# Performance work log

Hardware: AMD Instinct MI355X
Metric: run time of the kernel (lower is better)

The kernel has to match this reference:

```python
import jax, jax.numpy as jnp
import numpy as np

KERNELS = ("gaussian", "laplacian", "gaussian", "laplacian")
N, M, D, N_PER = 384, 384, 64, 200


def setup_inputs():
    key = jax.random.key(0)
    kx, ky, kb, kp = jax.random.split(key, 4)
    X = jax.random.normal(kx, (N, D), dtype=jnp.float32)
    Y = jax.random.normal(ky, (M, D), dtype=jnp.float32)
    # positive bandwidths of realistic magnitude for d=64 gaussian/laplacian kernels
    bandwidths = jax.random.uniform(kb, (4,), dtype=jnp.float32) * 8.0 + 4.0
    # each row is a random permutation of n+m indices (torch.randperm equivalent)
    perms = jax.vmap(lambda k: jax.random.permutation(k, N + M))(
        jax.random.split(kp, N_PER)).astype(jnp.int32)
    return {"X": X, "Y": Y, "bandwidths": bandwidths, "perms": perms}


def _pairwise_dist(Z):
    # torch.cdist(Z, Z, p=2); eps keeps sqrt grad finite on the zero diagonal
    sq = jnp.sum(Z * Z, axis=1)
    d2 = jnp.maximum(sq[:, None] + sq[None, :] - 2.0 * (Z @ Z.T), 0.0)
    return jnp.sqrt(d2 + 1e-12)


def reference(X, Y, bandwidths, perms):
    n, m = X.shape[0], Y.shape[0]
    Z = jnp.concatenate([X, Y], axis=0)            # [n+m, d]
    dist = _pairwise_dist(Z)                        # [n+m, n+m]
    idx = jnp.arange(min(n, m))
    perm_X, perm_Y = perms[:, :n], perms[:, n:]    # [n_per, n], [n_per, m]
    U, U_b = [], []
    for i, kern in enumerate(KERNELS):
        b = bandwidths[i]
        if kern == "gaussian":
            K = jnp.exp(-(dist * dist) / (b * b))
        else:  # laplacian
            K = jnp.exp(-dist / b)
        # mmd_u's in-place K_XY[diag]=0 mutates the view of K, so zero first
        K = K.at[idx, n + idx].set(0.0)
        K_XX, K_YY, K_XY = K[:n, :n], K[n:, n:], K[:n, n:]
        mmd = ((K_XX.sum() - jnp.trace(K_XX)) / (n * (n - 1))
               + (K_YY.sum() - jnp.trace(K_YY)) / (m * (m - 1))
               - 2.0 * K_XY.sum() / (n * m))
        U.append(mmd)
        # fast_perm: gather permuted blocks, zero diagonals, reduce per permutation
        diagK = jnp.diagonal(K)
        sXX = K[perm_X[:, :, None], perm_X[:, None, :]].sum((1, 2)) - diagK[perm_X].sum(1)
        sYY = K[perm_Y[:, :, None], perm_Y[:, None, :]].sum((1, 2)) - diagK[perm_Y].sum(1)
        sXY = (K[perm_X[:, :, None], perm_Y[:, None, :]].sum((1, 2))
               - K[perm_X[:, idx], perm_Y[:, idx]].sum(1))
        U_b.append(sXX / (n * (n - 1)) + sYY / (m * (m - 1)) - 2.0 * sXY / (n * m))
    U = jnp.stack(U)[:, None]    # [n_b, 1]  == compute_U_stats U.unsqueeze(1)
    U_b = jnp.stack(U_b)         # [n_b, n_per]
    return jnp.concatenate([U, U_b], axis=1)  # [n_b, 1 + n_per]
```

## Files before the change

### kernel.cpp

```cpp
#include <hip/hip_runtime.h>

#define NTOT 768
#define NHALF 384
#define DDIM 64
#define NPER 200
#define PPAD 256
#define NKER 4
#define CHUNK 192
#define NMB 12
#define NB_GEMM 192

typedef __attribute__((ext_vector_type(8))) short short8;
typedef __attribute__((ext_vector_type(4))) float floatx4;

constexpr int K0SZ  = NTOT * NTOT;
constexpr int OF_KH = 0;
constexpr int KH_FLOATS = NKER * K0SZ / 2;
constexpr int OF_RS0 = OF_KH + KH_FLOATS;
constexpr int OF_RSX = OF_RS0 + NKER * NTOT;
constexpr int OF_RSY = OF_RSX + NKER * NTOT;
constexpr int OF_C   = OF_RSY + NKER * NTOT;
constexpr int OF_ROWM = OF_C + NKER * NHALF;
constexpr int OF_COLM = OF_ROWM + NKER * NTOT;
constexpr int OF_SCAL = OF_COLM + NKER * NTOT;
constexpr int OF_STT  = OF_SCAL + 16;
constexpr int STT_FLOATS = PPAD * NTOT / 2;
constexpr int OF_Q0P  = OF_STT + STT_FLOATS;

constexpr int SMEMF = CHUNK * 65 + 2 * DDIM + 64;

__device__ __forceinline__ unsigned short f2bf(float f) {
    unsigned int u = __float_as_uint(f);
    return (unsigned short)((u + 0x7FFFu + ((u >> 16) & 1u)) >> 16);
}
__device__ __forceinline__ float bf2f(unsigned short h) {
    return __uint_as_float(((unsigned int)h) << 16);
}

__global__ __launch_bounds__(256) void k_s1(const float* __restrict__ X,
                                            const float* __restrict__ Y,
                                            const float* __restrict__ bw,
                                            const int* __restrict__ perms,
                                            float* __restrict__ ws) {
    __shared__ float smem[SMEMF];
    float* zb   = smem;
    float* zaS  = smem + CHUNK * 65;
    float* redw = zaS + 2 * DDIM;
    int bid = blockIdx.x, tid = threadIdx.x;
    int wave = tid >> 6, lane = tid & 63;
    unsigned short* STT = (unsigned short*)(ws + OF_STT);
    unsigned short* KH  = (unsigned short*)(ws + OF_KH);

    if (bid < NPER) {
        if (tid < 192) {
            ((uint2*)(STT + bid * NTOT))[tid] = make_uint2(0u, 0u);
            if (bid < PPAD - NPER)
                ((uint2*)(STT + (NPER + bid) * NTOT))[tid] = make_uint2(0u, 0u);
        }
        __syncthreads();
        int v = perms[bid * NTOT + tid];
        STT[bid * NTOT + v] = 0x3F80;
        if (tid < NHALF - 256) {
            int v2 = perms[bid * NTOT + 256 + tid];
            STT[bid * NTOT + v2] = 0x3F80;
        }
        return;
    }

    int a0 = bid - NPER;
    int a1 = a0 + NHALF;
    if (tid < DDIM)               zaS[tid] = X[a0 * DDIM + tid];
    else if (tid < 2 * DDIM)      zaS[tid] = Y[a0 * DDIM + (tid - DDIM)];
    float ib2[NKER], ib1[NKER];
#pragma unroll
    for (int k = 0; k < NKER; ++k) { float b = bw[k]; ib2[k] = 1.f / (b * b); ib1[k] = 1.f / b; }
    __syncthreads();
    float sq0 = 0.f, sq1 = 0.f;
#pragma unroll
    for (int d = 0; d < DDIM; ++d) {
        sq0 = fmaf(zaS[d], zaS[d], sq0);
        sq1 = fmaf(zaS[DDIM + d], zaS[DDIM + d], sq1);
    }
    float acc[16];
#pragma unroll
    for (int j = 0; j < 16; ++j) acc[j] = 0.f;

    for (int c0 = 0; c0 < NTOT; c0 += CHUNK) {
        __syncthreads();
        for (int idx = tid; idx < CHUNK * DDIM; idx += 256) {
            int r = idx >> 6, d = idx & 63;
            int gr = c0 + r;
            const float* zr = (gr < NHALF) ? X + gr * DDIM : Y + (gr - NHALF) * DDIM;
            zb[r * 65 + d] = zr[d];
        }
        __syncthreads();
        if (tid < CHUNK) {
            int b = c0 + tid;
            float dot0 = 0.f, dot1 = 0.f, sqb = 0.f;
#pragma unroll
            for (int d = 0; d < DDIM; ++d) {
                float zv = zb[tid * 65 + d];
                dot0 = fmaf(zaS[d], zv, dot0);
                dot1 = fmaf(zaS[DDIM + d], zv, dot1);
                sqb  = fmaf(zv, zv, sqb);
            }
            {
                float d2 = (sq0 + sqb) - 2.f * dot0;
                if (b == a0) d2 = 0.f;
                d2 = fmaxf(d2, 0.f);
                float d2e = d2 + 1e-12f;
                float dist = sqrtf(d2e);
#pragma unroll
                for (int k = 0; k < NKER; ++k) {
                    float val = ((k & 1) == 0) ? __expf(-d2e * ib2[k]) : __expf(-dist * ib1[k]);
                    KH[k * K0SZ + a0 * NTOT + b] = f2bf(val);
                    if (b < NHALF) acc[k] += val; else acc[4 + k] += val;
                    if (b == a0 + NHALF) ws[OF_C + k * NHALF + a0] = val;
                }
            }
            {
                float d2 = (sq1 + sqb) - 2.f * dot1;
                if (b == a1) d2 = 0.f;
                d2 = fmaxf(d2, 0.f);
                float d2e = d2 + 1e-12f;
                float dist = sqrtf(d2e);
#pragma unroll
                for (int k = 0; k < NKER; ++k) {
                    float val = ((k & 1) == 0) ? __expf(-d2e * ib2[k]) : __expf(-dist * ib1[k]);
                    KH[k * K0SZ + a1 * NTOT + b] = f2bf(val);
                    if (b < NHALF) acc[8 + k] += val; else acc[12 + k] += val;
                }
            }
        }
    }
#pragma unroll
    for (int off = 32; off > 0; off >>= 1)
#pragma unroll
        for (int j = 0; j < 16; ++j) acc[j] += __shfl_down(acc[j], off, 64);
    __syncthreads();
    if (lane == 0)
#pragma unroll
        for (int j = 0; j < 16; ++j) redw[wave * 16 + j] = acc[j];
    __syncthreads();
    if (tid == 0) {
#pragma unroll
        for (int k = 0; k < NKER; ++k) {
            float sx0 = redw[k]      + redw[16 + k]      + redw[32 + k]      + redw[48 + k];
            float sy0 = redw[4 + k]  + redw[20 + k]      + redw[36 + k]      + redw[52 + k];
            float sx1 = redw[8 + k]  + redw[24 + k]      + redw[40 + k]      + redw[56 + k];
            float sy1 = redw[12 + k] + redw[28 + k]      + redw[44 + k]      + redw[60 + k];
            ws[OF_RS0 + k * NTOT + a0] = sx0 + sy0;
            ws[OF_RSX + k * NTOT + a0] = sx0;
            ws[OF_RSY + k * NTOT + a0] = sy0;
            ws[OF_RS0 + k * NTOT + a1] = sx1 + sy1;
            ws[OF_RSX + k * NTOT + a1] = sx1;
            ws[OF_RSY + k * NTOT + a1] = sy1;
        }
    }
}

__global__ __launch_bounds__(256) void k_s2(const float* __restrict__ bw,
                                            float* __restrict__ ws, float* __restrict__ out) {
    __shared__ float smem[256];
    int bid = blockIdx.x, tid = threadIdx.x;
    int wave = tid >> 6, lane = tid & 63;

    if (bid < NB_GEMM) {
        int mb = bid % NMB;
        int t  = bid / NMB;
        int nc = t & 3;
        int k  = t >> 2;
        int m0 = mb * 64 + wave * 16;
        int n0 = nc * 64;
        int row = lane & 15, quad = lane >> 4;
        const unsigned short* KH  = (const unsigned short*)(ws + OF_KH);
        const unsigned short* STT = (const unsigned short*)(ws + OF_STT);
        const unsigned short* aptr = KH + k * K0SZ + (m0 + row) * NTOT + quad * 8;
        floatx4 acc[4][2];
#pragma unroll
        for (int j = 0; j < 4; ++j)
#pragma unroll
            for (int h = 0; h < 2; ++h) acc[j][h] = (floatx4){0.f, 0.f, 0.f, 0.f};
        for (int kk = 0; kk < NTOT; kk += 64) {
            short8 a0 = *(const short8*)(aptr + kk);
            short8 a1 = *(const short8*)(aptr + kk + 32);
#pragma unroll
            for (int j = 0; j < 4; ++j) {
                const unsigned short* bp = STT + (n0 + j * 16 + row) * NTOT + quad * 8 + kk;
                short8 b0 = *(const short8*)(bp);
                short8 b1 = *(const short8*)(bp + 32);
                acc[j][0] = __builtin_amdgcn_mfma_f32_16x16x32_bf16(a0, b0, acc[j][0], 0, 0, 0);
                acc[j][1] = __builtin_amdgcn_mfma_f32_16x16x32_bf16(a1, b1, acc[j][1], 0, 0, 0);
            }
        }
        __syncthreads();
#pragma unroll
        for (int j = 0; j < 4; ++j) {
            const unsigned short* sp = STT + (n0 + j * 16 + row) * NTOT + m0 + quad * 4;
            float p = 0.f;
#pragma unroll
            for (int r = 0; r < 4; ++r) p += (acc[j][0][r] + acc[j][1][r]) * bf2f(sp[r]);
            p += __shfl_down(p, 32, 64);
            p += __shfl_down(p, 16, 64);
            if (lane < 16) smem[wave * 64 + j * 16 + lane] = p;
        }
        __syncthreads();
        if (tid < 64) {
            float s = smem[tid] + smem[64 + tid] + smem[128 + tid] + smem[192 + tid];
            ws[OF_Q0P + (k * NMB + mb) * PPAD + n0 + tid] = s;
        }
        return;
    }

    int k = bid - NB_GEMM;
    float v[5] = {0.f, 0.f, 0.f, 0.f, 0.f};
    for (int a = tid; a < NTOT; a += 256) v[0] += ws[OF_RS0 + k * NTOT + a];
    for (int a = tid; a < NHALF; a += 256) {
        v[1] += ws[OF_C + k * NHALF + a];
        v[2] += ws[OF_RSX + k * NTOT + a];
        v[3] += ws[OF_RSY + k * NTOT + NHALF + a];
        v[4] += ws[OF_RSY + k * NTOT + a];
    }
#pragma unroll
    for (int off = 32; off > 0; off >>= 1)
#pragma unroll
        for (int j = 0; j < 5; ++j) v[j] += __shfl_down(v[j], off, 64);
    __syncthreads();
    if (lane == 0)
#pragma unroll
        for (int j = 0; j < 5; ++j) smem[wave * 8 + j] = v[j];
    __syncthreads();
    if (tid == 0) {
        float tot0 = smem[0] + smem[8] + smem[16] + smem[24];
        float csum = smem[1] + smem[9] + smem[17] + smem[25];
        float sxx  = smem[2] + smem[10] + smem[18] + smem[26];
        float syy  = smem[3] + smem[11] + smem[19] + smem[27];
        float sxy  = smem[4] + smem[12] + smem[20] + smem[28];
        float b = bw[k];
        float dist0 = sqrtf(1e-12f);
        float dk = ((k & 1) == 0) ? expf(-(dist0 * dist0) / (b * b)) : expf(-dist0 / b);
        ws[OF_SCAL + k * 4 + 0] = tot0 - csum;
        ws[OF_SCAL + k * 4 + 1] = dk;
        double U = ((double)sxx - 384.0 * (double)dk) * (1.0 / 147072.0)
                 + ((double)syy - 384.0 * (double)dk) * (1.0 / 147072.0)
                 - 2.0 * ((double)sxy - (double)csum) * (1.0 / 147456.0);
        out[k * 201] = (float)U;
    }
    for (int idx = tid; idx < NTOT; idx += 256) {
        float r0 = ws[OF_RS0 + k * NTOT + idx];
        float cx = (idx < NHALF)  ? ws[OF_C + k * NHALF + idx] : 0.f;
        float cy = (idx >= NHALF) ? ws[OF_C + k * NHALF + idx - NHALF] : 0.f;
        ws[OF_ROWM + k * NTOT + idx] = r0 - cx;
        ws[OF_COLM + k * NTOT + idx] = r0 - cy;
    }
}

__global__ __launch_bounds__(256) void k_s3(const int* __restrict__ perms,
                                            const float* __restrict__ ws,
                                            float* __restrict__ out) {
    __shared__ float smem[128];
    int p = blockIdx.x, tid = threadIdx.x;
    int wave = tid >> 6, lane = tid & 63;
    const unsigned short* STT = (const unsigned short*)(ws + OF_STT);
    const unsigned short* KH  = (const unsigned short*)(ws + OF_KH);
    float v[16] = {0.f};
    for (int i = tid; i < NHALF; i += 256) {
        int a  = perms[p * NTOT + i];
        int bY = perms[p * NTOT + NHALF + i];
        float si  = bf2f(STT[p * NTOT + i]);
        float si2 = bf2f(STT[p * NTOT + NHALF + i]);
#pragma unroll
        for (int k = 0; k < NKER; ++k) {
            v[k * 4 + 0] += ws[OF_ROWM + k * NTOT + a];
            v[k * 4 + 1] += ws[OF_COLM + k * NTOT + a];
            float kv = bf2f(KH[k * K0SZ + a * NTOT + bY]);
            if (a < NHALF && bY == a + NHALF) kv = 0.f;
            v[k * 4 + 2] += kv;
            v[k * 4 + 3] += ws[OF_C + k * NHALF + i] * si * si2;
        }
    }
#pragma unroll
    for (int off = 32; off > 0; off >>= 1)
#pragma unroll
        for (int j = 0; j < 16; ++j) v[j] += __shfl_down(v[j], off, 64);
    __syncthreads();
    if (lane == 0)
#pragma unroll
        for (int j = 0; j < 16; ++j) smem[wave * 16 + j] = v[j];
    __syncthreads();
    if (tid < 16) smem[64 + tid] = smem[tid] + smem[16 + tid] + smem[32 + tid] + smem[48 + tid];
    __syncthreads();
    if (tid < NKER) {
        int k = tid;
        double rs = smem[64 + k * 4 + 0], cs = smem[64 + k * 4 + 1];
        double pair = smem[64 + k * 4 + 2], qc = smem[64 + k * 4 + 3];
        double total_mod = (double)ws[OF_SCAL + k * 4 + 0];
        double dk        = (double)ws[OF_SCAL + k * 4 + 1];
        double q = -qc;
#pragma unroll
        for (int mb = 0; mb < NMB; ++mb) q += (double)ws[OF_Q0P + (k * NMB + mb) * PPAD + p];
        double sXX = q - 384.0 * dk;
        double sYY = total_mod - rs - cs + q - 384.0 * dk;
        double sXY = rs - q - pair;
        out[k * 201 + 1 + p] =
            (float)(sXX * (1.0 / 147072.0) + sYY * (1.0 / 147072.0) - 2.0 * sXY * (1.0 / 147456.0));
    }
}

extern "C" void kernel_launch(void* const* d_in, const int* in_sizes, int n_in,
                              void* d_out, int out_size, void* d_ws, size_t ws_size,
                              hipStream_t stream) {
    const float* X     = (const float*)d_in[0];
    const float* Y     = (const float*)d_in[1];
    const float* bw    = (const float*)d_in[2];
    const int*   perms = (const int*)d_in[3];
    float* ws  = (float*)d_ws;
    float* out = (float*)d_out;

    k_s1<<<NPER + NHALF, 256, 0, stream>>>(X, Y, bw, perms, ws);
    k_s2<<<NB_GEMM + NKER, 256, 0, stream>>>(bw, ws, out);
    k_s3<<<NPER, 256, 0, stream>>>(perms, ws, out);
}
```

Measured before the change: 113.0 us.

## Split kernel-matrix rows and GEMM K-dimension across more blocks

The distance/kernel stage now gives each block one row instead of two, so the grid doubles to 768 row blocks and each block needs fewer registers. The bilinear GEMM stage splits the reduction dimension into two halves, doubling the GEMM grid to 384 blocks. The final stage sums twice as many partial results. This raises parallelism and CU occupancy on a small problem, at the cost of more partial writes and redundant chunk loads of Z per block.

```diff
diff --git a/kernel.cpp b/kernel.cpp
--- a/kernel.cpp
+++ b/kernel.cpp
@@ -8,7 +8,9 @@
 #define NKER 4
 #define CHUNK 192
 #define NMB 12
-#define NB_GEMM 192
+#define NKH 2
+#define NB_GEMM 384
+#define NPART (NMB * NKH)
 
 typedef __attribute__((ext_vector_type(8))) short short8;
 typedef __attribute__((ext_vector_type(4))) float floatx4;
@@ -27,7 +29,7 @@
 constexpr int STT_FLOATS = PPAD * NTOT / 2;
 constexpr int OF_Q0P  = OF_STT + STT_FLOATS;
 
-constexpr int SMEMF = CHUNK * 65 + 2 * DDIM + 64;
+constexpr int SMEMF = CHUNK * 65 + DDIM + 32;
 
 __device__ __forceinline__ unsigned short f2bf(float f) {
     unsigned int u = __float_as_uint(f);
@@ -45,7 +47,7 @@
     __shared__ float smem[SMEMF];
     float* zb   = smem;
     float* zaS  = smem + CHUNK * 65;
-    float* redw = zaS + 2 * DDIM;
+    float* redw = zaS + DDIM;
     int bid = blockIdx.x, tid = threadIdx.x;
     int wave = tid >> 6, lane = tid & 63;
     unsigned short* STT = (unsigned short*)(ws + OF_STT);
@@ -67,23 +69,18 @@
         return;
     }
 
-    int a0 = bid - NPER;
-    int a1 = a0 + NHALF;
-    if (tid < DDIM)               zaS[tid] = X[a0 * DDIM + tid];
-    else if (tid < 2 * DDIM)      zaS[tid] = Y[a0 * DDIM + (tid - DDIM)];
+    int a = bid - NPER;
+    const float* za = (a < NHALF) ? X + a * DDIM : Y + (a - NHALF) * DDIM;
+    if (tid < DDIM) zaS[tid] = za[tid];
     float ib2[NKER], ib1[NKER];
 #pragma unroll
     for (int k = 0; k < NKER; ++k) { float b = bw[k]; ib2[k] = 1.f / (b * b); ib1[k] = 1.f / b; }
     __syncthreads();
-    float sq0 = 0.f, sq1 = 0.f;
-#pragma unroll
-    for (int d = 0; d < DDIM; ++d) {
-        sq0 = fmaf(zaS[d], zaS[d], sq0);
-        sq1 = fmaf(zaS[DDIM + d], zaS[DDIM + d], sq1);
-    }
-    float acc[16];
-#pragma unroll
-    for (int j = 0; j < 16; ++j) acc[j] = 0.f;
+    float sqa = 0.f;
+#pragma unroll
+    for (int d = 0; d < DDIM; ++d) sqa = fmaf(zaS[d], zaS[d], sqa);
+    float accX[NKER] = {0.f, 0.f, 0.f, 0.f};
+    float accY[NKER] = {0.f, 0.f, 0.f, 0.f};
 
     for (int c0 = 0; c0 < NTOT; c0 += CHUNK) {
         __syncthreads();
@@ -96,65 +93,47 @@
         __syncthreads();
         if (tid < CHUNK) {
             int b = c0 + tid;
-            float dot0 = 0.f, dot1 = 0.f, sqb = 0.f;
+            float dot = 0.f, sqb = 0.f;
 #pragma unroll
             for (int d = 0; d < DDIM; ++d) {
                 float zv = zb[tid * 65 + d];
-                dot0 = fmaf(zaS[d], zv, dot0);
-                dot1 = fmaf(zaS[DDIM + d], zv, dot1);
-                sqb  = fmaf(zv, zv, sqb);
+                dot = fmaf(zaS[d], zv, dot);
+                sqb = fmaf(zv, zv, sqb);
             }
-            {
-                float d2 = (sq0 + sqb) - 2.f * dot0;
-                if (b == a0) d2 = 0.f;
-                d2 = fmaxf(d2, 0.f);
-                float d2e = d2 + 1e-12f;
-                float dist = sqrtf(d2e);
-#pragma unroll
-                for (int k = 0; k < NKER; ++k) {
-                    float val = ((k & 1) == 0) ? __expf(-d2e * ib2[k]) : __expf(-dist * ib1[k]);
-                    KH[k * K0SZ + a0 * NTOT + b] = f2bf(val);
-                    if (b < NHALF) acc[k] += val; else acc[4 + k] += val;
-                    if (b == a0 + NHALF) ws[OF_C + k * NHALF + a0] = val;
-                }
+            float d2 = (sqa + sqb) - 2.f * dot;
+            if (b == a) d2 = 0.f;
+            d2 = fmaxf(d2, 0.f);
+            float d2e = d2 + 1e-12f;
+            float dist = sqrtf(d2e);
+#pragma unroll
+            for (int k = 0; k < NKER; ++k) {
+                float val = ((k & 1) == 0) ? __expf(-d2e * ib2[k]) : __expf(-dist * ib1[k]);
+                KH[k * K0SZ + a * NTOT + b] = f2bf(val);
+                if (b < NHALF) accX[k] += val; else accY[k] += val;
+                if (a < NHALF && b == a + NHALF) ws[OF_C + k * NHALF + a] = val;
             }
-            {
-                float d2 = (sq1 + sqb) - 2.f * dot1;
-                if (b == a1) d2 = 0.f;
-                d2 = fmaxf(d2, 0.f);
-                float d2e = d2 + 1e-12f;
-                float dist = sqrtf(d2e);
-#pragma unroll
-                for (int k = 0; k < NKER; ++k) {
-                    float val = ((k & 1) == 0) ? __expf(-d2e * ib2[k]) : __expf(-dist * ib1[k]);
-                    KH[k * K0SZ + a1 * NTOT + b] = f2bf(val);
-                    if (b < NHALF) acc[8 + k] += val; else acc[12 + k] += val;
-                }
-            }
-        }
-    }
+        }
+    }
+    float vals[8];
+#pragma unroll
+    for (int k = 0; k < NKER; ++k) { vals[k] = accX[k]; vals[4 + k] = accY[k]; }
 #pragma unroll
     for (int off = 32; off > 0; off >>= 1)
 #pragma unroll
-        for (int j = 0; j < 16; ++j) acc[j] += __shfl_down(acc[j], off, 64);
+        for (int v = 0; v < 8; ++v) vals[v] += __shfl_down(vals[v], off, 64);
     __syncthreads();
     if (lane == 0)
 #pragma unroll
-        for (int j = 0; j < 16; ++j) redw[wave * 16 + j] = acc[j];
+        for (int v = 0; v < 8; ++v) redw[wave * 8 + v] = vals[v];
     __syncthreads();
     if (tid == 0) {
 #pragma unroll
         for (int k = 0; k < NKER; ++k) {
-            float sx0 = redw[k]      + redw[16 + k]      + redw[32 + k]      + redw[48 + k];
-            float sy0 = redw[4 + k]  + redw[20 + k]      + redw[36 + k]      + redw[52 + k];
-            float sx1 = redw[8 + k]  + redw[24 + k]      + redw[40 + k]      + redw[56 + k];
-            float sy1 = redw[12 + k] + redw[28 + k]      + redw[44 + k]      + redw[60 + k];
-            ws[OF_RS0 + k * NTOT + a0] = sx0 + sy0;
-            ws[OF_RSX + k * NTOT + a0] = sx0;
-            ws[OF_RSY + k * NTOT + a0] = sy0;
-            ws[OF_RS0 + k * NTOT + a1] = sx1 + sy1;
-            ws[OF_RSX + k * NTOT + a1] = sx1;
-            ws[OF_RSY + k * NTOT + a1] = sy1;
+            float sx = redw[k] + redw[8 + k] + redw[16 + k] + redw[24 + k];
+            float sy = redw[4 + k] + redw[12 + k] + redw[20 + k] + redw[28 + k];
+            ws[OF_RS0 + k * NTOT + a] = sx + sy;
+            ws[OF_RSX + k * NTOT + a] = sx;
+            ws[OF_RSY + k * NTOT + a] = sy;
         }
     }
 }
@@ -169,7 +148,9 @@
         int mb = bid % NMB;
         int t  = bid / NMB;
         int nc = t & 3;
-        int k  = t >> 2;
+        int t2 = t >> 2;
+        int k  = t2 & 3;
+        int kh = t2 >> 2;
         int m0 = mb * 64 + wave * 16;
         int n0 = nc * 64;
         int row = lane & 15, quad = lane >> 4;
@@ -181,7 +162,8 @@
         for (int j = 0; j < 4; ++j)
 #pragma unroll
             for (int h = 0; h < 2; ++h) acc[j][h] = (floatx4){0.f, 0.f, 0.f, 0.f};
-        for (int kk = 0; kk < NTOT; kk += 64) {
+        int kk0 = kh * (NTOT / 2);
+        for (int kk = kk0; kk < kk0 + NTOT / 2; kk += 64) {
             short8 a0 = *(const short8*)(aptr + kk);
             short8 a1 = *(const short8*)(aptr + kk + 32);
 #pragma unroll
@@ -207,7 +189,7 @@
         __syncthreads();
         if (tid < 64) {
             float s = smem[tid] + smem[64 + tid] + smem[128 + tid] + smem[192 + tid];
-            ws[OF_Q0P + (k * NMB + mb) * PPAD + n0 + tid] = s;
+            ws[OF_Q0P + (k * NPART + kh * NMB + mb) * PPAD + n0 + tid] = s;
         }
         return;
     }
@@ -298,7 +280,7 @@
         double dk        = (double)ws[OF_SCAL + k * 4 + 1];
         double q = -qc;
 #pragma unroll
-        for (int mb = 0; mb < NMB; ++mb) q += (double)ws[OF_Q0P + (k * NMB + mb) * PPAD + p];
+        for (int j = 0; j < NPART; ++j) q += (double)ws[OF_Q0P + (k * NPART + j) * PPAD + p];
         double sXX = q - 384.0 * dk;
         double sYY = total_mod - rs - cs + q - 384.0 * dk;
         double sXY = rs - q - pair;
@@ -317,7 +299,7 @@
     float* ws  = (float*)d_ws;
     float* out = (float*)d_out;
 
-    k_s1<<<NPER + NHALF, 256, 0, stream>>>(X, Y, bw, perms, ws);
+    k_s1<<<NPER + NTOT, 256, 0, stream>>>(X, Y, bw, perms, ws);
     k_s2<<<NB_GEMM + NKER, 256, 0, stream>>>(bw, ws, out);
     k_s3<<<NPER, 256, 0, stream>>>(perms, ws, out);
 }
```

New measurement: 107.7 us. 1.05x faster.
